# Optimization experiments

Hardware: AMD Instinct MI355X
Metric: run time of the kernel (lower is better)

## Reference

```python
import jax, jax.numpy as jnp
import numpy as np

NUM_CONCEPTS = 4096
CONCEPT_DIM = 512


def setup_inputs() -> dict:
    key = jax.random.key(0)
    k1, k2 = jax.random.split(key)
    inp = jax.random.normal(k1, (8, 4096, CONCEPT_DIM), dtype=jnp.float32)
    bound = 1.0 / NUM_CONCEPTS
    codebook = jax.random.uniform(
        k2, (NUM_CONCEPTS, CONCEPT_DIM), dtype=jnp.float32,
        minval=-bound, maxval=bound)
    return {"inp": inp, "codebook": codebook}


def reference(inp, codebook):
    # flatten tokens: [N, D]
    flat = inp.reshape(-1, inp.shape[-1])
    # squared Euclidean distances [N, K]; argmin is identical to cdist argmin
    d2 = (
        jnp.sum(flat * flat, axis=1, keepdims=True)
        - 2.0 * jnp.einsum("nd,kd->nk", flat, codebook)
        + jnp.sum(codebook * codebook, axis=1)[None, :]
    )
    idx = jnp.argmin(d2, axis=1)  # [N]
    quantized = jnp.take(codebook, idx, axis=0).reshape(inp.shape)
    return quantized
```

## Files before the change

kernel.cpp:

```cpp
#include <hip/hip_runtime.h>
#include <math.h>

constexpr int D  = 512;
constexpr int K  = 4096;
constexpr int BM = 64;
constexpr int BN = 64;
constexpr int BD_LEG = 32;
constexpr int PAD = 4;

#define MARGIN 2.5e-3f
constexpr int RCAP = 12;
constexpr unsigned CAPQ = 8388608u;

typedef short short8v __attribute__((ext_vector_type(8)));
typedef float f32x4   __attribute__((ext_vector_type(4)));

constexpr size_t SC_OFF   = 0;
constexpr size_t SX_OFF   = 16384;
constexpr size_t KEYS_OFF = SX_OFF + 131072;
constexpr size_t QCNT_OFF = KEYS_OFF + 262144;
constexpr size_t CBP_OFF  = QCNT_OFF + 4096;
constexpr size_t WS_NEED  = CBP_OFF + (size_t)K * D * 2;

__device__ inline unsigned short rne_bf16(float x) {
    unsigned u = __float_as_uint(x);
    return (unsigned short)((u + 0x7FFFu + ((u >> 16) & 1u)) >> 16);
}
__device__ inline unsigned ordkey(float f) {
    unsigned u = __float_as_uint(f);
    return (u & 0x80000000u) ? ~u : (u | 0x80000000u);
}
__device__ inline float fromkey(unsigned k) {
    unsigned u = (k & 0x80000000u) ? (k ^ 0x80000000u) : ~k;
    return __uint_as_float(u);
}
__device__ inline void gload16(const void* g, void* l) {
    __builtin_amdgcn_global_load_lds(
        (const __attribute__((address_space(1))) unsigned*)g,
        (__attribute__((address_space(3))) unsigned*)l, 16, 0, 0);
}

__global__ __launch_bounds__(256)
void prep_kernel(const float* __restrict__ cb, const float* __restrict__ inp,
                 float* __restrict__ sc, unsigned short* __restrict__ cbp,
                 float* __restrict__ sxg, unsigned short* __restrict__ ap,
                 int nb_cb) {
    const int t = threadIdx.x;
    if ((int)blockIdx.x < nb_cb) {
        {
            const int row  = blockIdx.x * 4 + (t >> 6);
            const int lane = t & 63;
            const float* r = cb + (size_t)row * D + lane * 8;
            float4 v0 = *(const float4*)r;
            float4 v1 = *(const float4*)(r + 4);
            float s = v0.x * v0.x;
            s += v0.y * v0.y; s += v0.z * v0.z; s += v0.w * v0.w;
            s += v1.x * v1.x; s += v1.y * v1.y; s += v1.z * v1.z; s += v1.w * v1.w;
#pragma unroll
            for (int off = 1; off < 64; off <<= 1) s += __shfl_xor(s, off, 64);
            if (lane == 0) sc[row] = s;
        }
        {
            const int s   = blockIdx.x * 256 + t;
            const int tile = s >> 14;
            const int db  = (s >> 10) & 15;
            const int j   = (s >> 8) & 3;
            const int row = s & 255;
            const float* sp = cb + (size_t)(tile * 256 + row) * D + db * 32 + j * 8;
            float4 v0 = *(const float4*)sp;
            float4 v1 = *(const float4*)(sp + 4);
            float xs[8] = {v0.x, v0.y, v0.z, v0.w, v1.x, v1.y, v1.z, v1.w};
            union { short8v v; unsigned short u[8]; } H;
#pragma unroll
            for (int i = 0; i < 8; ++i) H.u[i] = rne_bf16(xs[i]);
            *(short8v*)(cbp + (size_t)s * 8) = H.v;
        }
    } else {
        const int m0 = ((int)blockIdx.x - nb_cb) * 64;
        const int r  = t >> 2, p = t & 3;
        const int row  = m0 + r;
        const int tile = row >> 7;
        const int rit  = row & 127;
        const float* rowp = inp + (size_t)row * D + p * 128;
        unsigned short* dbase = ap + ((size_t)tile * 8192 + (size_t)(p * 4) * 512 + rit) * 8;
        float s = 0.0f;
#pragma unroll
        for (int g = 0; g < 16; ++g) {
            float4 v0 = *(const float4*)(rowp + g * 8);
            float4 v1 = *(const float4*)(rowp + g * 8 + 4);
            s = fmaf(v0.x, v0.x, s); s = fmaf(v0.y, v0.y, s);
            s = fmaf(v0.z, v0.z, s); s = fmaf(v0.w, v0.w, s);
            s = fmaf(v1.x, v1.x, s); s = fmaf(v1.y, v1.y, s);
            s = fmaf(v1.z, v1.z, s); s = fmaf(v1.w, v1.w, s);
            float xs[8] = {v0.x, v0.y, v0.z, v0.w, v1.x, v1.y, v1.z, v1.w};
            union { short8v v; unsigned short u[8]; } H;
#pragma unroll
            for (int i = 0; i < 8; ++i) H.u[i] = rne_bf16(xs[i]);
            *(short8v*)(dbase + ((size_t)(g >> 2) * 512 + (size_t)(g & 3) * 128) * 8) = H.v;
        }
        s += __shfl_xor(s, 1, 64);
        s += __shfl_xor(s, 2, 64);
        if (p == 0) sxg[row] = s;
    }
}

__device__ float exact_dot512(const float* __restrict__ x, const float* __restrict__ c) {
    float s = 0.0f;
#pragma unroll 4
    for (int i = 0; i < 128; ++i) {
        const float4 xv = *(const float4*)(x + i * 4);
        const float4 cv = *(const float4*)(c + i * 4);
        s = fmaf(xv.x, cv.x, s); s = fmaf(xv.y, cv.y, s);
        s = fmaf(xv.z, cv.z, s); s = fmaf(xv.w, cv.w, s);
    }
    return s;
}

__global__ __launch_bounds__(512)
void score_kernel(const unsigned short* __restrict__ a_perm,
                  const unsigned short* __restrict__ b_perm,
                  const float* __restrict__ sc,
                  char* __restrict__ records) {
    __shared__ __align__(16) unsigned short lds[2 * 12288];
    __shared__ unsigned minsh[128];
    __shared__ unsigned cntsh[128];
    __shared__ unsigned short listsh[128][RCAP];

    const int t    = threadIdx.x;
    const int lane = t & 63;
    const int w    = t >> 6;
    const int wm   = w >> 2;
    const int wn   = w & 3;
    const int l15  = lane & 15;
    const int lk   = lane >> 4;
    const int bm   = blockIdx.x >> 4;
    const int bn   = blockIdx.x & 15;

    const unsigned short* gA = a_perm + (size_t)bm * 65536  + (size_t)t * 8;
    const unsigned short* gB = b_perm + (size_t)bn * 131072 + (size_t)t * 8;

    if (t < 128) { minsh[t] = 0xFFFFFFFFu; cntsh[t] = 0u; }

    f32x4 acc[4][4];
#pragma unroll
    for (int i = 0; i < 4; ++i)
#pragma unroll
        for (int j = 0; j < 4; ++j) acc[i][j] = f32x4{0.f, 0.f, 0.f, 0.f};

    auto STAGE = [&](int sa, int sb, int dbuf) {
        gload16(gA + sa,        &lds[dbuf + (w * 64) * 8]);
        gload16(gB + sb,        &lds[dbuf + 4096 + (0 * 512 + w * 64) * 8]);
        gload16(gB + sb + 4096, &lds[dbuf + 4096 + (1 * 512 + w * 64) * 8]);
    };

    STAGE(0, 0, 0);
    __syncthreads();

    const unsigned short* lbA = &lds[lk * 1024 + l15 * 8];
    const unsigned short* lbB = &lds[4096 + lk * 2048 + l15 * 8];
    const int mbase = wm * 512;
    const int nbase = wn * 512;

    auto COMPUTE = [&](int cur) {
        short8v af[4], bf[4];
#pragma unroll
        for (int mt = 0; mt < 4; ++mt)
            af[mt] = *(const short8v*)(lbA + cur + mbase + mt * 128);
#pragma unroll
        for (int nt = 0; nt < 4; ++nt)
            bf[nt] = *(const short8v*)(lbB + cur + nbase + nt * 128);
#pragma unroll
        for (int mt = 0; mt < 4; ++mt)
#pragma unroll
            for (int nt = 0; nt < 4; ++nt)
                acc[mt][nt] = __builtin_amdgcn_mfma_f32_16x16x32_bf16(af[mt], bf[nt], acc[mt][nt], 0, 0, 0);
    };

    int sa = 4096, sb = 8192;
#pragma unroll 1
    for (int p = 0; p < 8; ++p) {
        STAGE(sa, sb, 12288); sa += 4096; sb += 8192;
        COMPUTE(0);
        __syncthreads();
        if (p < 7) { STAGE(sa, sb, 0); sa += 4096; sb += 8192; }
        COMPUTE(12288);
        __syncthreads();
    }

    float scv[4];
#pragma unroll
    for (int nt = 0; nt < 4; ++nt) scv[nt] = sc[bn * 256 + wn * 64 + nt * 16 + l15];

#pragma unroll
    for (int mt = 0; mt < 4; ++mt)
#pragma unroll
        for (int nt = 0; nt < 4; ++nt)
#pragma unroll
            for (int r = 0; r < 4; ++r)
                acc[mt][nt][r] = fmaf(-2.0f, acc[mt][nt][r], scv[nt]);

#pragma unroll
    for (int mt = 0; mt < 4; ++mt)
#pragma unroll
        for (int r = 0; r < 4; ++r) {
            float m4 = fminf(fminf(acc[mt][0][r], acc[mt][1][r]),
                             fminf(acc[mt][2][r], acc[mt][3][r]));
            m4 = fminf(m4, __shfl_xor(m4, 1, 64));
            m4 = fminf(m4, __shfl_xor(m4, 2, 64));
            m4 = fminf(m4, __shfl_xor(m4, 4, 64));
            m4 = fminf(m4, __shfl_xor(m4, 8, 64));
            if (l15 == 0) {
                const int tok = wm * 64 + mt * 16 + lk * 4 + r;
                atomicMin(&minsh[tok], ordkey(m4));
            }
        }
    __syncthreads();

#pragma unroll
    for (int mt = 0; mt < 4; ++mt)
#pragma unroll
        for (int r = 0; r < 4; ++r) {
            const int tok = wm * 64 + mt * 16 + lk * 4 + r;
            const float tmn = fromkey(minsh[tok]) + MARGIN;
#pragma unroll
            for (int nt = 0; nt < 4; ++nt) {
                if (acc[mt][nt][r] <= tmn) {
                    unsigned p = atomicAdd(&cntsh[tok], 1u);
                    if (p < RCAP)
                        listsh[tok][p] = (unsigned short)(bn * 256 + wn * 64 + nt * 16 + l15);
                }
            }
        }
    __syncthreads();

    if (t < 128) {
        const unsigned* lw = (const unsigned*)&listsh[t][0];
        uint4 r0, r1;
        r0.x = __float_as_uint(fromkey(minsh[t]));
        r0.y = cntsh[t];
        r0.z = lw[0]; r0.w = lw[1];
        r1.x = lw[2]; r1.y = lw[3]; r1.z = lw[4]; r1.w = lw[5];
        char* rp = records + ((size_t)(bm * 128 + t) * 16 + bn) * 32;
        *(uint4*)rp = r0;
        *(uint4*)(rp + 16) = r1;
    }
}

__global__ __launch_bounds__(256)
void compact_kernel(const char* __restrict__ records,
                    unsigned long long* __restrict__ keysg,
                    unsigned* __restrict__ qcnt,
                    unsigned* __restrict__ queue) {
    const int token = blockIdx.x * 256 + threadIdx.x;
    keysg[token] = 0xFFFFFFFFFFFFFFFFull;

    const char* rbase = records + (size_t)token * 16 * 32;
    float mn = __builtin_huge_valf();
#pragma unroll
    for (int i = 0; i < 16; ++i)
        mn = fminf(mn, *(const float*)(rbase + (size_t)i * 32));
    const float thr = mn + MARGIN;

    unsigned my = 0;
#pragma unroll 1
    for (int i = 0; i < 16; ++i) {
        const char* rp = rbase + (size_t)i * 32;
        if (*(const float*)rp <= thr) {
            const unsigned cnt = *(const unsigned*)(rp + 4);
            my += (cnt <= RCAP) ? cnt : 256u;
        }
    }
    unsigned pos = atomicAdd(qcnt, my);
#pragma unroll 1
    for (int i = 0; i < 16; ++i) {
        const char* rp = rbase + (size_t)i * 32;
        if (*(const float*)rp <= thr) {
            const unsigned cnt = *(const unsigned*)(rp + 4);
            if (cnt <= RCAP) {
                const unsigned short* cs = (const unsigned short*)(rp + 8);
                for (unsigned j = 0; j < cnt; ++j) {
                    if (pos < CAPQ) queue[pos] = ((unsigned)token << 12) | cs[j];
                    ++pos;
                }
            } else {
                for (int c2 = 0; c2 < 256; ++c2) {
                    if (pos < CAPQ) queue[pos] = ((unsigned)token << 12) | (unsigned)(i * 256 + c2);
                    ++pos;
                }
            }
        }
    }
}

__global__ __launch_bounds__(256)
void exec_kernel(const float* __restrict__ inp, const float* __restrict__ cb,
                 const float* __restrict__ sc, const float* __restrict__ sxg,
                 const unsigned* __restrict__ qcnt, const unsigned* __restrict__ queue,
                 unsigned long long* __restrict__ keysg, int nblk64) {
    const unsigned raw = *qcnt;
    unsigned total = raw > CAPQ ? CAPQ : raw;
    const unsigned stride = gridDim.x * 256;
    for (unsigned i = blockIdx.x * 256 + threadIdx.x; i < total; i += stride) {
        const unsigned e = queue[i];
        const int token = e >> 12;
        const int code  = e & 4095;
        const float dot = exact_dot512(inp + (size_t)token * D, cb + (size_t)code * D);
        const float tmp = sxg[token] - 2.0f * dot;
        const float v   = tmp + sc[code];
        const unsigned long long key =
            ((unsigned long long)__float_as_uint(v) << 32) | (unsigned)code;
        atomicMin(&keysg[token], key);
    }
    if (raw > CAPQ && blockIdx.x < (unsigned)nblk64) {
        const int t = threadIdx.x;
        const int m0 = blockIdx.x * 64;
#pragma unroll 1
        for (int tok = 0; tok < 64; ++tok) {
            const int token = m0 + tok;
            const float sxv = sxg[token];
            const float* xrow = inp + (size_t)token * D;
            for (int code = t; code < K; code += 256) {
                const float dot = exact_dot512(xrow, cb + (size_t)code * D);
                const float tmp = sxv - 2.0f * dot;
                const float v   = tmp + sc[code];
                const unsigned long long key =
                    ((unsigned long long)__float_as_uint(v) << 32) | (unsigned)code;
                atomicMin(&keysg[token], key);
            }
        }
    }
}

__global__ __launch_bounds__(256)
void gather_kernel(const float* __restrict__ cb,
                   const unsigned long long* __restrict__ keysg,
                   float* __restrict__ out) {
    const int m0 = blockIdx.x * 64;
    __shared__ int bidx[64];
    if (threadIdx.x < 64) bidx[threadIdx.x] = (int)(keysg[m0 + threadIdx.x] & 0xFFFFFFFFull);
    __syncthreads();
    for (int q = threadIdx.x; q < 64 * (D / 4); q += 256) {
        const int r = q >> 7;
        const int c = (q & 127) * 4;
        *(float4*)(out + (size_t)(m0 + r) * D + c) = *(const float4*)(cb + (size_t)bidx[r] * D + c);
    }
}

__global__ __launch_bounds__(256)
void sc_kernel(const float* __restrict__ cb, float* __restrict__ sc) {
    const int row  = blockIdx.x * 4 + (threadIdx.x >> 6);
    const int lane = threadIdx.x & 63;
    const float* r = cb + (size_t)row * D + lane * 8;
    float4 v0 = *(const float4*)r;
    float4 v1 = *(const float4*)(r + 4);
    float s = v0.x * v0.x;
    s += v0.y * v0.y; s += v0.z * v0.z; s += v0.w * v0.w;
    s += v1.x * v1.x; s += v1.y * v1.y; s += v1.z * v1.z; s += v1.w * v1.w;
#pragma unroll
    for (int off = 1; off < 64; off <<= 1) s += __shfl_xor(s, off, 64);
    if (lane == 0) sc[row] = s;
}

__global__ __launch_bounds__(256)
void vq_kernel(const float* __restrict__ inp, const float* __restrict__ cb,
               const float* __restrict__ sc, float* __restrict__ out) {
    __shared__ __align__(16) float As[BD_LEG][BM + PAD];
    __shared__ __align__(16) float Bs[BD_LEG][BN + PAD];
    __shared__ float sxl[BM];
    __shared__ float scs[BN];
    __shared__ int   bidx[BM];

    const int t  = threadIdx.x;
    const int m0 = blockIdx.x * BM;
    const int tm = t >> 4;
    const int tn = t & 15;
    const float FINF = __builtin_huge_valf();

    {
        const int r = t >> 2, p = t & 3;
        const float* row = inp + (size_t)(m0 + r) * D + p * 128;
        float s = 0.0f;
#pragma unroll
        for (int i = 0; i < 32; ++i) {
            float4 v = *(const float4*)(row + i * 4);
            s = fmaf(v.x, v.x, s); s = fmaf(v.y, v.y, s);
            s = fmaf(v.z, v.z, s); s = fmaf(v.w, v.w, s);
        }
        s += __shfl_xor(s, 1, 64);
        s += __shfl_xor(s, 2, 64);
        if (p == 0) sxl[r] = s;
    }
    __syncthreads();

    float sxm[4];
#pragma unroll
    for (int i = 0; i < 4; ++i) sxm[i] = sxl[tm * 4 + i];

    float runv[4] = {FINF, FINF, FINF, FINF};
    int   runi[4] = {0, 0, 0, 0};
    const int dq = (t & 7) << 2;
    const int mr = t >> 3;

#pragma unroll 1
    for (int kb = 0; kb < K; kb += BN) {
        __syncthreads();
        if (t < BN) scs[t] = sc[kb + t];

        float accl[4][4];
#pragma unroll
        for (int i = 0; i < 4; ++i)
#pragma unroll
            for (int j = 0; j < 4; ++j) accl[i][j] = 0.0f;

#pragma unroll 1
        for (int db = 0; db < D; db += BD_LEG) {
            const float* ap = inp + (size_t)(m0 + mr) * D + db + dq;
            const float* bp = cb  + (size_t)(kb + mr) * D + db + dq;
            float4 av0 = *(const float4*)ap;
            float4 av1 = *(const float4*)(ap + (size_t)32 * D);
            float4 bv0 = *(const float4*)bp;
            float4 bv1 = *(const float4*)(bp + (size_t)32 * D);
            __syncthreads();
            As[dq + 0][mr] = av0.x; As[dq + 1][mr] = av0.y;
            As[dq + 2][mr] = av0.z; As[dq + 3][mr] = av0.w;
            As[dq + 0][mr + 32] = av1.x; As[dq + 1][mr + 32] = av1.y;
            As[dq + 2][mr + 32] = av1.z; As[dq + 3][mr + 32] = av1.w;
            Bs[dq + 0][mr] = bv0.x; Bs[dq + 1][mr] = bv0.y;
            Bs[dq + 2][mr] = bv0.z; Bs[dq + 3][mr] = bv0.w;
            Bs[dq + 0][mr + 32] = bv1.x; Bs[dq + 1][mr + 32] = bv1.y;
            Bs[dq + 2][mr + 32] = bv1.z; Bs[dq + 3][mr + 32] = bv1.w;
            __syncthreads();
#pragma unroll
            for (int d = 0; d < BD_LEG; ++d) {
                const float4 a = *(const float4*)(&As[d][tm * 4]);
                const float4 b = *(const float4*)(&Bs[d][tn * 4]);
                float af[4] = {a.x, a.y, a.z, a.w};
                float bf[4] = {b.x, b.y, b.z, b.w};
#pragma unroll
                for (int i = 0; i < 4; ++i)
#pragma unroll
                    for (int j = 0; j < 4; ++j)
                        accl[i][j] = fmaf(af[i], bf[j], accl[i][j]);
            }
        }
#pragma unroll
        for (int i = 0; i < 4; ++i) {
            float bv = FINF;
            int   bi = 0x7fffffff;
#pragma unroll
            for (int j = 0; j < 4; ++j) {
                const float p = accl[i][j];
                const float tmp = sxm[i] - 2.0f * p;
                const float v   = tmp + scs[tn * 4 + j];
                const int  idx  = kb + tn * 4 + j;
                if (v < bv) { bv = v; bi = idx; }
            }
#pragma unroll
            for (int off = 1; off < 16; off <<= 1) {
                const float ov = __shfl_xor(bv, off, 64);
                const int   oi = __shfl_xor(bi, off, 64);
                if (ov < bv || (ov == bv && oi < bi)) { bv = ov; bi = oi; }
            }
            if (bv < runv[i]) { runv[i] = bv; runi[i] = bi; }
        }
    }
    if (tn == 0) {
#pragma unroll
        for (int i = 0; i < 4; ++i) bidx[tm * 4 + i] = runi[i];
    }
    __syncthreads();
#pragma unroll 1
    for (int q = t; q < BM * (D / 4); q += 256) {
        const int r = q >> 7;
        const int c = (q & 127) * 4;
        const float4 v = *(const float4*)(cb + (size_t)bidx[r] * D + c);
        *(float4*)(out + (size_t)(m0 + r) * D + c) = v;
    }
}

extern "C" void kernel_launch(void* const* d_in, const int* in_sizes, int n_in,
                              void* d_out, int out_size, void* d_ws, size_t ws_size,
                              hipStream_t stream) {
    const float* inp = (const float*)d_in[0];
    const float* cb  = (const float*)d_in[1];
    float* out = (float*)d_out;
    float* sc  = (float*)d_ws;
    const int tokens = in_sizes[0] / D;

    const bool fast = (ws_size >= WS_NEED) && (tokens % 256 == 0) &&
                      (in_sizes[1] == K * D) &&
                      ((size_t)out_size * 4 >= (size_t)tokens * D * 2 + (size_t)tokens * 16 * 32);

    if (fast) {
        float* sxg = (float*)((char*)d_ws + SX_OFF);
        unsigned long long* keysg = (unsigned long long*)((char*)d_ws + KEYS_OFF);
        unsigned* qcnt = (unsigned*)((char*)d_ws + QCNT_OFF);
        unsigned short* cbp = (unsigned short*)((char*)d_ws + CBP_OFF);
        unsigned short* ap  = (unsigned short*)d_out;
        char* records = (char*)d_out + (size_t)tokens * D * 2;
        unsigned* queue = (unsigned*)d_out;

        const int nb_cb = K / 4;

        hipMemsetAsync(qcnt, 0, sizeof(unsigned), stream);
        prep_kernel<<<nb_cb + tokens / 64, 256, 0, stream>>>(cb, inp, sc, cbp, sxg, ap, nb_cb);
        score_kernel<<<(tokens / 128) * 16, 512, 0, stream>>>(ap, cbp, sc, records);
        compact_kernel<<<tokens / 256, 256, 0, stream>>>(records, keysg, qcnt, queue);
        exec_kernel<<<2048, 256, 0, stream>>>(inp, cb, sc, sxg, qcnt, queue, keysg, tokens / 64);
        gather_kernel<<<tokens / 64, 256, 0, stream>>>(cb, keysg, out);
    } else {
        sc_kernel<<<K / 4, 256, 0, stream>>>(cb, sc);
        vq_kernel<<<tokens / BM, 256, 0, stream>>>(inp, cb, sc, out);
    }
}
```

Baseline: 320.9 us.

## Switch candidate-screening GEMM from bf16 to int8 MFMA with per-row scales

The prep kernel now quantizes both codebook and input rows to symmetric int8 with per-row absmax scales, instead of converting them to bf16. The score kernel uses the i32 16x16x64 int8 MFMA and dequantizes with the product of the two row scales before the margin-based candidate filter. This halves operand bytes and doubles MFMA K-depth per instruction, aiming to cut screening GEMM time. The queue-counter memset is folded into prep_kernel, removing one launch. The risk is that coarser int8 scores could push the true nearest code outside the fixed margin, or enlarge candidate lists, before the exact fp32 rescoring step.

After: 286.9 us. -10.6%, faster.

```diff
diff --git a/kernel.cpp b/kernel.cpp
--- a/kernel.cpp
+++ b/kernel.cpp
@@ -10,22 +10,21 @@
 
 #define MARGIN 2.5e-3f
 constexpr int RCAP = 12;
-constexpr unsigned CAPQ = 8388608u;
+constexpr unsigned CAPQ = 4194304u;
 
 typedef short short8v __attribute__((ext_vector_type(8)));
 typedef float f32x4   __attribute__((ext_vector_type(4)));
+typedef int   int4v   __attribute__((ext_vector_type(4)));
 
 constexpr size_t SC_OFF   = 0;
 constexpr size_t SX_OFF   = 16384;
-constexpr size_t KEYS_OFF = SX_OFF + 131072;
-constexpr size_t QCNT_OFF = KEYS_OFF + 262144;
-constexpr size_t CBP_OFF  = QCNT_OFF + 4096;
-constexpr size_t WS_NEED  = CBP_OFF + (size_t)K * D * 2;
-
-__device__ inline unsigned short rne_bf16(float x) {
-    unsigned u = __float_as_uint(x);
-    return (unsigned short)((u + 0x7FFFu + ((u >> 16) & 1u)) >> 16);
-}
+constexpr size_t KEYS_OFF = 147456;
+constexpr size_t QCNT_OFF = 409600;
+constexpr size_t SCS_OFF  = 413696;
+constexpr size_t SXS_OFF  = 430080;
+constexpr size_t CBP_OFF  = 561152;
+constexpr size_t WS_NEED  = CBP_OFF + (size_t)K * D;
+
 __device__ inline unsigned ordkey(float f) {
     unsigned u = __float_as_uint(f);
     return (u & 0x80000000u) ? ~u : (u | 0x80000000u);
@@ -42,65 +41,69 @@
 
 __global__ __launch_bounds__(256)
 void prep_kernel(const float* __restrict__ cb, const float* __restrict__ inp,
-                 float* __restrict__ sc, unsigned short* __restrict__ cbp,
-                 float* __restrict__ sxg, unsigned short* __restrict__ ap,
-                 int nb_cb) {
+                 float* __restrict__ sc, float* __restrict__ scs,
+                 unsigned char* __restrict__ cbp,
+                 float* __restrict__ sxg, float* __restrict__ sxs,
+                 unsigned char* __restrict__ ap,
+                 unsigned* __restrict__ qcnt, int nb_cb) {
     const int t = threadIdx.x;
-    if ((int)blockIdx.x < nb_cb) {
-        {
-            const int row  = blockIdx.x * 4 + (t >> 6);
-            const int lane = t & 63;
-            const float* r = cb + (size_t)row * D + lane * 8;
-            float4 v0 = *(const float4*)r;
-            float4 v1 = *(const float4*)(r + 4);
-            float s = v0.x * v0.x;
-            s += v0.y * v0.y; s += v0.z * v0.z; s += v0.w * v0.w;
-            s += v1.x * v1.x; s += v1.y * v1.y; s += v1.z * v1.z; s += v1.w * v1.w;
-#pragma unroll
-            for (int off = 1; off < 64; off <<= 1) s += __shfl_xor(s, off, 64);
-            if (lane == 0) sc[row] = s;
-        }
-        {
-            const int s   = blockIdx.x * 256 + t;
-            const int tile = s >> 14;
-            const int db  = (s >> 10) & 15;
-            const int j   = (s >> 8) & 3;
-            const int row = s & 255;
-            const float* sp = cb + (size_t)(tile * 256 + row) * D + db * 32 + j * 8;
-            float4 v0 = *(const float4*)sp;
-            float4 v1 = *(const float4*)(sp + 4);
-            float xs[8] = {v0.x, v0.y, v0.z, v0.w, v1.x, v1.y, v1.z, v1.w};
-            union { short8v v; unsigned short u[8]; } H;
-#pragma unroll
-            for (int i = 0; i < 8; ++i) H.u[i] = rne_bf16(xs[i]);
-            *(short8v*)(cbp + (size_t)s * 8) = H.v;
-        }
-    } else {
-        const int m0 = ((int)blockIdx.x - nb_cb) * 64;
-        const int r  = t >> 2, p = t & 3;
-        const int row  = m0 + r;
-        const int tile = row >> 7;
-        const int rit  = row & 127;
-        const float* rowp = inp + (size_t)row * D + p * 128;
-        unsigned short* dbase = ap + ((size_t)tile * 8192 + (size_t)(p * 4) * 512 + rit) * 8;
-        float s = 0.0f;
-#pragma unroll
-        for (int g = 0; g < 16; ++g) {
-            float4 v0 = *(const float4*)(rowp + g * 8);
-            float4 v1 = *(const float4*)(rowp + g * 8 + 4);
-            s = fmaf(v0.x, v0.x, s); s = fmaf(v0.y, v0.y, s);
-            s = fmaf(v0.z, v0.z, s); s = fmaf(v0.w, v0.w, s);
-            s = fmaf(v1.x, v1.x, s); s = fmaf(v1.y, v1.y, s);
-            s = fmaf(v1.z, v1.z, s); s = fmaf(v1.w, v1.w, s);
-            float xs[8] = {v0.x, v0.y, v0.z, v0.w, v1.x, v1.y, v1.z, v1.w};
-            union { short8v v; unsigned short u[8]; } H;
-#pragma unroll
-            for (int i = 0; i < 8; ++i) H.u[i] = rne_bf16(xs[i]);
-            *(short8v*)(dbase + ((size_t)(g >> 2) * 512 + (size_t)(g & 3) * 128) * 8) = H.v;
-        }
-        s += __shfl_xor(s, 1, 64);
-        s += __shfl_xor(s, 2, 64);
-        if (p == 0) sxg[row] = s;
+    if (blockIdx.x == 0 && t == 0) *qcnt = 0u;
+    const bool isCB = (int)blockIdx.x < nb_cb;
+    const int r = t >> 2, p = t & 3;
+    const int row = (isCB ? (int)blockIdx.x : ((int)blockIdx.x - nb_cb)) * 64 + r;
+    const float* base = (isCB ? cb : inp) + (size_t)row * D + p * 128;
+
+    float s = 0.0f, m = 0.0f;
+#pragma unroll
+    for (int g = 0; g < 16; ++g) {
+        float4 v0 = *(const float4*)(base + g * 8);
+        float4 v1 = *(const float4*)(base + g * 8 + 4);
+        s = fmaf(v0.x, v0.x, s); s = fmaf(v0.y, v0.y, s);
+        s = fmaf(v0.z, v0.z, s); s = fmaf(v0.w, v0.w, s);
+        s = fmaf(v1.x, v1.x, s); s = fmaf(v1.y, v1.y, s);
+        s = fmaf(v1.z, v1.z, s); s = fmaf(v1.w, v1.w, s);
+        m = fmaxf(m, fmaxf(fmaxf(fabsf(v0.x), fabsf(v0.y)), fmaxf(fabsf(v0.z), fabsf(v0.w))));
+        m = fmaxf(m, fmaxf(fmaxf(fabsf(v1.x), fabsf(v1.y)), fmaxf(fabsf(v1.z), fabsf(v1.w))));
+    }
+    s += __shfl_xor(s, 1, 64);
+    s += __shfl_xor(s, 2, 64);
+    m = fmaxf(m, __shfl_xor(m, 1, 64));
+    m = fmaxf(m, __shfl_xor(m, 2, 64));
+    const float sinv  = (m > 0.0f) ? 127.0f / m : 0.0f;
+    const float scale = m * (1.0f / 127.0f);
+    if (p == 0) {
+        if (isCB) { sc[row] = s;  scs[row] = scale; }
+        else      { sxg[row] = s; sxs[row] = scale; }
+    }
+
+    const int rstride = isCB ? 256 : 128;
+    const int tile    = isCB ? (row >> 8) : (row >> 7);
+    const int rit     = isCB ? (row & 255) : (row & 127);
+    unsigned char* dst = isCB ? cbp : ap;
+    const size_t tbase = (size_t)tile * (32 * rstride);
+#pragma unroll
+    for (int g = 0; g < 16; ++g) {
+        float4 v0 = *(const float4*)(base + g * 8);
+        float4 v1 = *(const float4*)(base + g * 8 + 4);
+        float xs[8] = {v0.x, v0.y, v0.z, v0.w, v1.x, v1.y, v1.z, v1.w};
+        unsigned u0 = 0, u1 = 0;
+#pragma unroll
+        for (int i = 0; i < 4; ++i) {
+            int q = (int)rintf(xs[i] * sinv);
+            q = q > 127 ? 127 : (q < -127 ? -127 : q);
+            u0 |= ((unsigned)(q & 255)) << (8 * i);
+        }
+#pragma unroll
+        for (int i = 4; i < 8; ++i) {
+            int q = (int)rintf(xs[i] * sinv);
+            q = q > 127 ? 127 : (q < -127 ? -127 : q);
+            u1 |= ((unsigned)(q & 255)) << (8 * (i - 4));
+        }
+        const int db = 2 * p + (g >> 3);
+        const int j  = ((16 * p + g) >> 1) & 3;
+        const size_t slot = tbase + (size_t)db * (4 * rstride) + (size_t)j * rstride + rit;
+        *(unsigned*)(dst + slot * 16 + (g & 1) * 8)     = u0;
+        *(unsigned*)(dst + slot * 16 + (g & 1) * 8 + 4) = u1;
     }
 }
 
@@ -117,11 +120,12 @@
 }
 
 __global__ __launch_bounds__(512)
-void score_kernel(const unsigned short* __restrict__ a_perm,
-                  const unsigned short* __restrict__ b_perm,
-                  const float* __restrict__ sc,
+void score_kernel(const unsigned char* __restrict__ a_perm,
+                  const unsigned char* __restrict__ b_perm,
+                  const float* __restrict__ sc, const float* __restrict__ scs,
+                  const float* __restrict__ sxs,
                   char* __restrict__ records) {
-    __shared__ __align__(16) unsigned short lds[2 * 12288];
+    __shared__ __align__(16) unsigned char lds[2 * 24576];
     __shared__ unsigned minsh[128];
     __shared__ unsigned cntsh[128];
     __shared__ unsigned short listsh[128][RCAP];
@@ -136,81 +140,95 @@
     const int bm   = blockIdx.x >> 4;
     const int bn   = blockIdx.x & 15;
 
-    const unsigned short* gA = a_perm + (size_t)bm * 65536  + (size_t)t * 8;
-    const unsigned short* gB = b_perm + (size_t)bn * 131072 + (size_t)t * 8;
+    const unsigned char* gA = a_perm + (size_t)bm * 65536  + (size_t)t * 16;
+    const unsigned char* gB = b_perm + (size_t)bn * 131072 + (size_t)t * 16;
 
     if (t < 128) { minsh[t] = 0xFFFFFFFFu; cntsh[t] = 0u; }
 
-    f32x4 acc[4][4];
+    int4v acc[4][4];
 #pragma unroll
     for (int i = 0; i < 4; ++i)
 #pragma unroll
-        for (int j = 0; j < 4; ++j) acc[i][j] = f32x4{0.f, 0.f, 0.f, 0.f};
-
-    auto STAGE = [&](int sa, int sb, int dbuf) {
-        gload16(gA + sa,        &lds[dbuf + (w * 64) * 8]);
-        gload16(gB + sb,        &lds[dbuf + 4096 + (0 * 512 + w * 64) * 8]);
-        gload16(gB + sb + 4096, &lds[dbuf + 4096 + (1 * 512 + w * 64) * 8]);
+        for (int j = 0; j < 4; ++j) acc[i][j] = int4v{0, 0, 0, 0};
+
+    auto STAGE = [&](int db, int dbuf) {
+        gload16(gA + (size_t)db * 8192,         &lds[dbuf + t * 16]);
+        gload16(gB + (size_t)db * 16384,        &lds[dbuf + 8192 + t * 16]);
+        gload16(gB + (size_t)db * 16384 + 8192, &lds[dbuf + 16384 + t * 16]);
     };
 
-    STAGE(0, 0, 0);
+    STAGE(0, 0);
     __syncthreads();
 
-    const unsigned short* lbA = &lds[lk * 1024 + l15 * 8];
-    const unsigned short* lbB = &lds[4096 + lk * 2048 + l15 * 8];
-    const int mbase = wm * 512;
-    const int nbase = wn * 512;
+    const unsigned char* lbA = &lds[lk * 2048 + l15 * 16];
+    const unsigned char* lbB = &lds[8192 + lk * 4096 + l15 * 16];
+    const int mbase = wm * 1024;
+    const int nbase = wn * 1024;
 
     auto COMPUTE = [&](int cur) {
-        short8v af[4], bf[4];
+        int4v af[4], bf[4];
 #pragma unroll
         for (int mt = 0; mt < 4; ++mt)
-            af[mt] = *(const short8v*)(lbA + cur + mbase + mt * 128);
+            af[mt] = *(const int4v*)(lbA + cur + mbase + mt * 256);
 #pragma unroll
         for (int nt = 0; nt < 4; ++nt)
-            bf[nt] = *(const short8v*)(lbB + cur + nbase + nt * 128);
+            bf[nt] = *(const int4v*)(lbB + cur + nbase + nt * 256);
 #pragma unroll
         for (int mt = 0; mt < 4; ++mt)
 #pragma unroll
             for (int nt = 0; nt < 4; ++nt)
-                acc[mt][nt] = __builtin_amdgcn_mfma_f32_16x16x32_bf16(af[mt], bf[nt], acc[mt][nt], 0, 0, 0);
+                acc[mt][nt] = __builtin_amdgcn_mfma_i32_16x16x64_i8(af[mt], bf[nt], acc[mt][nt], 0, 0, 0);
     };
 
-    int sa = 4096, sb = 8192;
-#pragma unroll 1
-    for (int p = 0; p < 8; ++p) {
-        STAGE(sa, sb, 12288); sa += 4096; sb += 8192;
+    int sdb = 1;
+#pragma unroll 1
+    for (int p = 0; p < 4; ++p) {
+        STAGE(sdb, 24576); ++sdb;
         COMPUTE(0);
         __syncthreads();
-        if (p < 7) { STAGE(sa, sb, 0); sa += 4096; sb += 8192; }
-        COMPUTE(12288);
+        if (p < 3) { STAGE(sdb, 0); ++sdb; }
+        COMPUTE(24576);
         __syncthreads();
     }
 
-    float scv[4];
-#pragma unroll
-    for (int nt = 0; nt < 4; ++nt) scv[nt] = sc[bn * 256 + wn * 64 + nt * 16 + l15];
-
+    float scvv[4], scsv[4];
+#pragma unroll
+    for (int nt = 0; nt < 4; ++nt) {
+        const int code = bn * 256 + wn * 64 + nt * 16 + l15;
+        scvv[nt] = sc[code];
+        scsv[nt] = scs[code];
+    }
+    float sxsv[4][4];
 #pragma unroll
     for (int mt = 0; mt < 4; ++mt)
 #pragma unroll
+        for (int rr = 0; rr < 4; ++rr)
+            sxsv[mt][rr] = sxs[bm * 128 + wm * 64 + mt * 16 + lk * 4 + rr];
+
+#pragma unroll
+    for (int mt = 0; mt < 4; ++mt)
+#pragma unroll
         for (int nt = 0; nt < 4; ++nt)
 #pragma unroll
-            for (int r = 0; r < 4; ++r)
-                acc[mt][nt][r] = fmaf(-2.0f, acc[mt][nt][r], scv[nt]);
+            for (int rr = 0; rr < 4; ++rr) {
+                const float df = (float)acc[mt][nt][rr];
+                const float vv = fmaf(-2.0f * sxsv[mt][rr] * scsv[nt], df, scvv[nt]);
+                acc[mt][nt][rr] = __float_as_int(vv);
+            }
+#define VACC(mt, nt, rr) __int_as_float(acc[mt][nt][rr])
 
 #pragma unroll
     for (int mt = 0; mt < 4; ++mt)
 #pragma unroll
-        for (int r = 0; r < 4; ++r) {
-            float m4 = fminf(fminf(acc[mt][0][r], acc[mt][1][r]),
-                             fminf(acc[mt][2][r], acc[mt][3][r]));
+        for (int rr = 0; rr < 4; ++rr) {
+            float m4 = fminf(fminf(VACC(mt, 0, rr), VACC(mt, 1, rr)),
+                             fminf(VACC(mt, 2, rr), VACC(mt, 3, rr)));
             m4 = fminf(m4, __shfl_xor(m4, 1, 64));
             m4 = fminf(m4, __shfl_xor(m4, 2, 64));
             m4 = fminf(m4, __shfl_xor(m4, 4, 64));
             m4 = fminf(m4, __shfl_xor(m4, 8, 64));
             if (l15 == 0) {
-                const int tok = wm * 64 + mt * 16 + lk * 4 + r;
+                const int tok = wm * 64 + mt * 16 + lk * 4 + rr;
                 atomicMin(&minsh[tok], ordkey(m4));
             }
         }
@@ -219,12 +237,12 @@
 #pragma unroll
     for (int mt = 0; mt < 4; ++mt)
 #pragma unroll
-        for (int r = 0; r < 4; ++r) {
-            const int tok = wm * 64 + mt * 16 + lk * 4 + r;
+        for (int rr = 0; rr < 4; ++rr) {
+            const int tok = wm * 64 + mt * 16 + lk * 4 + rr;
             const float tmn = fromkey(minsh[tok]) + MARGIN;
 #pragma unroll
             for (int nt = 0; nt < 4; ++nt) {
-                if (acc[mt][nt][r] <= tmn) {
+                if (VACC(mt, nt, rr) <= tmn) {
                     unsigned p = atomicAdd(&cntsh[tok], 1u);
                     if (p < RCAP)
                         listsh[tok][p] = (unsigned short)(bn * 256 + wn * 64 + nt * 16 + l15);
@@ -232,6 +250,7 @@
             }
         }
     __syncthreads();
+#undef VACC
 
     if (t < 128) {
         const unsigned* lw = (const unsigned*)&listsh[t][0];
@@ -367,7 +386,7 @@
     __shared__ __align__(16) float As[BD_LEG][BM + PAD];
     __shared__ __align__(16) float Bs[BD_LEG][BN + PAD];
     __shared__ float sxl[BM];
-    __shared__ float scs[BN];
+    __shared__ float scs_l[BN];
     __shared__ int   bidx[BM];
 
     const int t  = threadIdx.x;
@@ -404,7 +423,7 @@
 #pragma unroll 1
     for (int kb = 0; kb < K; kb += BN) {
         __syncthreads();
-        if (t < BN) scs[t] = sc[kb + t];
+        if (t < BN) scs_l[t] = sc[kb + t];
 
         float accl[4][4];
 #pragma unroll
@@ -451,7 +470,7 @@
             for (int j = 0; j < 4; ++j) {
                 const float p = accl[i][j];
                 const float tmp = sxm[i] - 2.0f * p;
-                const float v   = tmp + scs[tn * 4 + j];
+                const float v   = tmp + scs_l[tn * 4 + j];
                 const int  idx  = kb + tn * 4 + j;
                 if (v < bv) { bv = v; bi = idx; }
             }
@@ -489,22 +508,24 @@
 
     const bool fast = (ws_size >= WS_NEED) && (tokens % 256 == 0) &&
                       (in_sizes[1] == K * D) &&
-                      ((size_t)out_size * 4 >= (size_t)tokens * D * 2 + (size_t)tokens * 16 * 32);
+                      ((size_t)out_size * 4 >= (size_t)tokens * D + (size_t)tokens * 16 * 32);
 
     if (fast) {
         float* sxg = (float*)((char*)d_ws + SX_OFF);
         unsigned long long* keysg = (unsigned long long*)((char*)d_ws + KEYS_OFF);
         unsigned* qcnt = (unsigned*)((char*)d_ws + QCNT_OFF);
-        unsigned short* cbp = (unsigned short*)((char*)d_ws + CBP_OFF);
-        unsigned short* ap  = (unsigned short*)d_out;
-        char* records = (char*)d_out + (size_t)tokens * D * 2;
+        float* scsg = (float*)((char*)d_ws + SCS_OFF);
+        float* sxsg = (float*)((char*)d_ws + SXS_OFF);
+        unsigned char* cbp = (unsigned char*)((char*)d_ws + CBP_OFF);
+        unsigned char* ap  = (unsigned char*)d_out;
+        char* records = (char*)d_out + (size_t)tokens * D;
         unsigned* queue = (unsigned*)d_out;
 
-        const int nb_cb = K / 4;
-
-        hipMemsetAsync(qcnt, 0, sizeof(unsigned), stream);
-        prep_kernel<<<nb_cb + tokens / 64, 256, 0, stream>>>(cb, inp, sc, cbp, sxg, ap, nb_cb);
-        score_kernel<<<(tokens / 128) * 16, 512, 0, stream>>>(ap, cbp, sc, records);
+        const int nb_cb = K / 64;
+
+        prep_kernel<<<nb_cb + tokens / 64, 256, 0, stream>>>(cb, inp, sc, scsg, cbp,
+                                                             sxg, sxsg, ap, qcnt, nb_cb);
+        score_kernel<<<(tokens / 128) * 16, 512, 0, stream>>>(ap, cbp, sc, scsg, sxsg, records);
         compact_kernel<<<tokens / 256, 256, 0, stream>>>(records, keysg, qcnt, queue);
         exec_kernel<<<2048, 256, 0, stream>>>(inp, cb, sc, sxg, qcnt, queue, keysg, tokens / 64);
         gather_kernel<<<tokens / 64, 256, 0, stream>>>(cb, keysg, out);
```
